# Kernel tuning notes

Hardware: AMD Instinct MI355X
Metric: run time of the kernel (lower is better)

The kernel has to match this reference:

```python
import jax, jax.numpy as jnp
import numpy as np

B, C, L, D = 8, 256, 2048, 128  # batch, in_channels, seq_len, n_factor


def setup_inputs() -> dict:
    key = jax.random.key(0)
    ks = jax.random.split(key, 8)
    s = 1.0 / np.sqrt(C)
    return {
        "x_inner": jax.random.normal(ks[0], (B, C, L), jnp.float32),
        "x_outer": jax.random.normal(ks[1], (B, C, L), jnp.float32),
        "Wq": jax.random.normal(ks[2], (D, C), jnp.float32) * s,
        "bq": jax.random.normal(ks[3], (D,), jnp.float32) * 0.01,
        "Wk": jax.random.normal(ks[4], (D, C), jnp.float32) * s,
        "bk": jax.random.normal(ks[5], (D,), jnp.float32) * 0.01,
        "Wv": jax.random.normal(ks[6], (D, C), jnp.float32) * s,
        "bv": jax.random.normal(ks[7], (D,), jnp.float32) * 0.01,
    }


def reference(x_inner, x_outer, Wq, bq, Wk, bk, Wv, bv):
    # kernel-size-1 Conv1d == per-position linear over channels; permute -> [B, L, D]
    q = jnp.einsum('bcl,dc->bld', x_inner, Wq) + bq  # [B, Lq, D]
    k = jnp.einsum('bcl,dc->bld', x_outer, Wk) + bk  # [B, Lk, D]
    v = jnp.einsum('bcl,dc->bld', x_outer, Wv) + bv  # [B, Lk, D]
    scores = jnp.einsum('bqd,bkd->bqk', q, k) / jnp.sqrt(jnp.asarray(D, q.dtype))
    attn = jax.nn.softmax(scores, axis=2)            # [B, Lq, Lk]
    return jnp.einsum('bqk,bkd->bqd', attn, v)       # [B, Lq, D]
```

## Files before the change

kernel.cpp:

```cpp
#include <hip/hip_runtime.h>
#include <hip/hip_bf16.h>

#define NB 8
#define NC 256
#define NL 2048
#define ND 128
#define NROWS (NB * NL)
#define QKV_ELEMS ((size_t)NB * NL * ND)
#define W_ELEMS (ND * NC)
#define XS_STRIDE 264

typedef __attribute__((ext_vector_type(8))) short bf16x8;
typedef __attribute__((ext_vector_type(4))) float f32x4;
typedef __attribute__((ext_vector_type(16))) float f32x16;

__device__ __forceinline__ unsigned short f2bf(float f) {
    union { float f; unsigned u; } v; v.f = f;
    unsigned r = v.u + 0x7fffu + ((v.u >> 16) & 1u);
    return (unsigned short)(r >> 16);
}

__device__ __forceinline__ void load_lds16(const unsigned short* g, unsigned short* l) {
    __builtin_amdgcn_global_load_lds((const __attribute__((address_space(1))) unsigned int*)g,
                                     (__attribute__((address_space(3))) unsigned int*)l, 16, 0, 0);
}

__global__ void cast_w3(const float* __restrict__ wq, const float* __restrict__ wk,
                        const float* __restrict__ wv, unsigned short* __restrict__ dst) {
    int i = blockIdx.x * blockDim.x + threadIdx.x;
    if (i >= 3 * W_ELEMS) return;
    int sel = i / W_ELEMS, off = i - sel * W_ELEMS;
    const float* s = (sel == 0) ? wq : (sel == 1) ? wk : wv;
    dst[i] = f2bf(s[off]);
}

__global__ __launch_bounds__(256, 4) void proj_direct(const float* __restrict__ xi,
                                                      const float* __restrict__ xo,
                                                      const unsigned short* __restrict__ Wall,
                                                      const float* __restrict__ bq,
                                                      const float* __restrict__ bk,
                                                      const float* __restrict__ bv,
                                                      unsigned short* __restrict__ Qb,
                                                      unsigned short* __restrict__ Kb,
                                                      unsigned short* __restrict__ Vtb) {
    __shared__ unsigned short xs[64 * XS_STRIDE];
    int b = blockIdx.x >> 5, lt = blockIdx.x & 31, l0 = lt * 64;
    int y = blockIdx.y;
    int wave = threadIdx.x >> 6, lane = threadIdx.x & 63;
    int ln = lane & 15, quad = lane >> 4;

    const float* xsrc = (y == 0 ? xi : xo) + (size_t)b * NC * NL + l0;
    int l4 = (lane & 15) * 4;
    int cr0 = wave * 4 + (lane >> 4);
    #pragma unroll
    for (int g = 0; g < 4; g++) {
        float4 r[4];
        #pragma unroll
        for (int gi = 0; gi < 4; gi++) {
            int c = cr0 + (g * 4 + gi) * 16;
            r[gi] = *reinterpret_cast<const float4*>(xsrc + (size_t)c * NL + l4);
        }
        #pragma unroll
        for (int gi = 0; gi < 4; gi++) {
            int c = cr0 + (g * 4 + gi) * 16;
            xs[(l4 + 0) * XS_STRIDE + c] = f2bf(r[gi].x);
            xs[(l4 + 1) * XS_STRIDE + c] = f2bf(r[gi].y);
            xs[(l4 + 2) * XS_STRIDE + c] = f2bf(r[gi].z);
            xs[(l4 + 3) * XS_STRIDE + c] = f2bf(r[gi].w);
        }
    }
    __syncthreads();

    if (y < 2) {
        const unsigned short* Wb = Wall + (size_t)y * W_ELEMS;
        const float* bias = y ? bk : bq;
        unsigned short* out = y ? Kb : Qb;
        int m0w = wave * 16;
        f32x4 acc[8] = {};
        #pragma unroll
        for (int s = 0; s < 8; s++) {
            bf16x8 af = *reinterpret_cast<const bf16x8*>(xs + (m0w + ln) * XS_STRIDE + s * 32 + quad * 8);
            #pragma unroll
            for (int t = 0; t < 8; t++) {
                bf16x8 bfr = *reinterpret_cast<const bf16x8*>(Wb + (size_t)(t * 16 + ln) * NC + s * 32 + quad * 8);
                acc[t] = __builtin_amdgcn_mfma_f32_16x16x32_bf16(af, bfr, acc[t], 0, 0, 0);
            }
        }
        #pragma unroll
        for (int t = 0; t < 8; t++) {
            int col = t * 16 + ln;
            float bi = bias[col];
            #pragma unroll
            for (int r = 0; r < 4; r++)
                out[(size_t)(b * NL + l0 + m0w + quad * 4 + r) * ND + col] = f2bf(acc[t][r] + bi);
        }
    } else {
        const unsigned short* Wb = Wall + 2 * (size_t)W_ELEMS;
        f32x4 acc[2][4] = {};
        #pragma unroll
        for (int s = 0; s < 8; s++) {
            bf16x8 wf0 = *reinterpret_cast<const bf16x8*>(Wb + (size_t)(wave * 32 + ln) * NC + s * 32 + quad * 8);
            bf16x8 wf1 = *reinterpret_cast<const bf16x8*>(Wb + (size_t)(wave * 32 + 16 + ln) * NC + s * 32 + quad * 8);
            #pragma unroll
            for (int t = 0; t < 4; t++) {
                bf16x8 xb = *reinterpret_cast<const bf16x8*>(xs + (t * 16 + ln) * XS_STRIDE + s * 32 + quad * 8);
                acc[0][t] = __builtin_amdgcn_mfma_f32_16x16x32_bf16(wf0, xb, acc[0][t], 0, 0, 0);
                acc[1][t] = __builtin_amdgcn_mfma_f32_16x16x32_bf16(wf1, xb, acc[1][t], 0, 0, 0);
            }
        }
        #pragma unroll
        for (int u = 0; u < 2; u++)
            #pragma unroll
            for (int t = 0; t < 4; t++)
                #pragma unroll
                for (int r = 0; r < 4; r++) {
                    int d = wave * 32 + u * 16 + quad * 4 + r;
                    Vtb[(size_t)(b * ND + d) * NL + l0 + t * 16 + ln] = f2bf(acc[u][t][r] + bv[d]);
                }
    }
}

__global__ __launch_bounds__(256, 2) void flash_attn_split(const unsigned short* __restrict__ Q,
                                                           const unsigned short* __restrict__ K,
                                                           const unsigned short* __restrict__ Vt,
                                                           float* __restrict__ Opart,
                                                           float* __restrict__ lbuf,
                                                           int kvlen) {
    __shared__ unsigned short kbuf[2][64 * 128];
    __shared__ unsigned short vbuf[2][128 * 64];
    __shared__ unsigned short pbuf[4][32 * 64];
    int b = blockIdx.x >> 4, qt = blockIdx.x & 15;
    int sp = blockIdx.y;
    int kv0 = sp * kvlen;
    int wave = threadIdx.x >> 6, lane = threadIdx.x & 63;
    int l31 = lane & 31, h = lane >> 5;
    int m0 = qt * 128 + wave * 32;
    const float scale = 0.08838834764831845f * 1.4426950408889634f;

    bf16x8 qf[8];
    const unsigned short* qrow = Q + (size_t)(b * NL + m0 + l31) * ND + h * 8;
    #pragma unroll
    for (int s = 0; s < 8; s++) qf[s] = *reinterpret_cast<const bf16x8*>(qrow + s * 16);

    float lsum = 0.f;
    f32x16 o_acc[4] = {};

    unsigned short* pw = pbuf[wave];
    const unsigned short* kg = K + (size_t)b * NL * ND;
    const unsigned short* vg = Vt + (size_t)b * ND * NL;

    int krt = wave * 16 + (lane >> 4);
    int kjs = (lane & 15);
    int vdt = wave * 32 + (lane >> 3);
    int vjs = (lane & 7);

    {
        int kt = kv0;
        #pragma unroll
        for (int i = 0; i < 4; i++) {
            int rt = krt + i * 4;
            load_lds16(kg + (size_t)(kt + rt) * ND + (kjs ^ (rt & 15)) * 8, kbuf[0] + (wave * 16 + i * 4) * 128);
        }
        #pragma unroll
        for (int i = 0; i < 4; i++) {
            int dt = vdt + i * 8;
            load_lds16(vg + (size_t)dt * NL + kt + (vjs ^ (dt & 7)) * 8, vbuf[0] + (wave * 32 + i * 8) * 64);
        }
    }

    int niter = kvlen >> 6;
    for (int it = 0; it < niter; it++) {
        int cur = it & 1;
        __syncthreads();

        if (it + 1 < niter) {
            int kt = kv0 + (it + 1) * 64;
            int nxt = cur ^ 1;
            #pragma unroll
            for (int i = 0; i < 4; i++) {
                int rt = krt + i * 4;
                load_lds16(kg + (size_t)(kt + rt) * ND + (kjs ^ (rt & 15)) * 8, kbuf[nxt] + (wave * 16 + i * 4) * 128);
            }
            #pragma unroll
            for (int i = 0; i < 4; i++) {
                int dt = vdt + i * 8;
                load_lds16(vg + (size_t)dt * NL + kt + (vjs ^ (dt & 7)) * 8, vbuf[nxt] + (wave * 32 + i * 8) * 64);
            }
        }
        const unsigned short* kb = kbuf[cur];
        const unsigned short* vb = vbuf[cur];

        f32x16 sacc[2] = {};
        #pragma unroll
        for (int tt = 0; tt < 2; tt++) {
            const unsigned short* krow_p = kb + (tt * 32 + l31) * 128;
            #pragma unroll
            for (int s = 0; s < 8; s++) {
                bf16x8 kf = *reinterpret_cast<const bf16x8*>(krow_p + (((s * 2 + h) ^ (lane & 15)) << 3));
                sacc[tt] = __builtin_amdgcn_mfma_f32_32x32x16_bf16(kf, qf[s], sacc[tt], 0, 0, 0);
            }
        }
        #pragma unroll
        for (int tt = 0; tt < 2; tt++) {
            #pragma unroll
            for (int g = 0; g < 4; g++) {
                float p0 = __builtin_exp2f(sacc[tt][g * 4 + 0] * scale);
                float p1 = __builtin_exp2f(sacc[tt][g * 4 + 1] * scale);
                float p2 = __builtin_exp2f(sacc[tt][g * 4 + 2] * scale);
                float p3 = __builtin_exp2f(sacc[tt][g * 4 + 3] * scale);
                lsum += (p0 + p1) + (p2 + p3);
                ushort4 o4 = { f2bf(p0), f2bf(p1), f2bf(p2), f2bf(p3) };
                int chunk = tt * 4 + g;
                *reinterpret_cast<ushort4*>(pw + l31 * 64 + ((chunk ^ (l31 & 7)) << 3) + h * 4) = o4;
            }
        }
        bf16x8 pb[4];
        #pragma unroll
        for (int step = 0; step < 4; step++)
            pb[step] = *reinterpret_cast<const bf16x8*>(pw + l31 * 64 + (((step * 2 + h) ^ (l31 & 7)) << 3));
        #pragma unroll
        for (int dt = 0; dt < 4; dt++) {
            const unsigned short* vrow = vb + (dt * 32 + l31) * 64;
            #pragma unroll
            for (int step = 0; step < 4; step++) {
                bf16x8 vf = *reinterpret_cast<const bf16x8*>(vrow + (((step * 2 + h) ^ (l31 & 7)) << 3));
                o_acc[dt] = __builtin_amdgcn_mfma_f32_32x32x16_bf16(vf, pb[step], o_acc[dt], 0, 0, 0);
            }
        }
    }
    lsum += __shfl_xor(lsum, 32);

    float* op = Opart + (size_t)sp * QKV_ELEMS;
    int qrow_g = b * NL + m0 + l31;
    if (lane < 32) lbuf[(size_t)sp * NROWS + qrow_g] = lsum;
    #pragma unroll
    for (int dt = 0; dt < 4; dt++) {
        #pragma unroll
        for (int g = 0; g < 4; g++) {
            f32x4 v4 = { o_acc[dt][g * 4 + 0], o_acc[dt][g * 4 + 1],
                         o_acc[dt][g * 4 + 2], o_acc[dt][g * 4 + 3] };
            *reinterpret_cast<f32x4*>(op + (size_t)qrow_g * ND + dt * 32 + g * 8 + h * 4) = v4;
        }
    }
}

__global__ __launch_bounds__(256) void attn_merge(const float* __restrict__ Opart,
                                                  const float* __restrict__ lbuf,
                                                  float* __restrict__ out, int S) {
    int idx = blockIdx.x * 256 + threadIdx.x;
    int row = idx >> 5;
    int dg = (idx & 31) * 4;
    float L = 0.f;
    float4 acc = make_float4(0.f, 0.f, 0.f, 0.f);
    for (int s = 0; s < S; s++) {
        L += lbuf[(size_t)s * NROWS + row];
        float4 o = *reinterpret_cast<const float4*>(Opart + (size_t)s * QKV_ELEMS + (size_t)row * ND + dg);
        acc.x += o.x; acc.y += o.y; acc.z += o.z; acc.w += o.w;
    }
    float inv = 1.0f / L;
    float4 res = make_float4(acc.x * inv, acc.y * inv, acc.z * inv, acc.w * inv);
    *reinterpret_cast<float4*>(out + (size_t)row * ND + dg) = res;
}

extern "C" void kernel_launch(void* const* d_in, const int* in_sizes, int n_in,
                              void* d_out, int out_size, void* d_ws, size_t ws_size,
                              hipStream_t stream) {
    const float* x_inner = (const float*)d_in[0];
    const float* x_outer = (const float*)d_in[1];
    const float* Wq = (const float*)d_in[2];
    const float* bq = (const float*)d_in[3];
    const float* Wk = (const float*)d_in[4];
    const float* bk = (const float*)d_in[5];
    const float* Wv = (const float*)d_in[6];
    const float* bv = (const float*)d_in[7];
    float* out = (float*)d_out;

    size_t need4 = 34078720u + 3 * QKV_ELEMS * 2 + 3 * W_ELEMS * 2;
    int S = (ws_size >= need4) ? 4 : 2;
    size_t union_bytes = (S == 4) ? 34078720u : 17039360u;

    char* w = (char*)d_ws;
    float* Opart = (float*)w;
    float* lbuf = (float*)(w + (size_t)S * QKV_ELEMS * 4);
    unsigned short* Qb = (unsigned short*)(w + union_bytes);
    unsigned short* Kb = Qb + QKV_ELEMS;
    unsigned short* Vtb = Kb + QKV_ELEMS;
    unsigned short* Wall = Vtb + QKV_ELEMS;

    cast_w3<<<(3 * W_ELEMS + 255) / 256, 256, 0, stream>>>(Wq, Wk, Wv, Wall);
    dim3 pgrid(NB * (NL / 64), 3);
    proj_direct<<<pgrid, 256, 0, stream>>>(x_inner, x_outer, Wall, bq, bk, bv, Qb, Kb, Vtb);
    dim3 fgrid(NB * (NL / 128), S);
    flash_attn_split<<<fgrid, 256, 0, stream>>>(Qb, Kb, Vtb, Opart, lbuf, NL / S);
    attn_merge<<<(NROWS * ND / 4 + 255) / 256, 256, 0, stream>>>(Opart, lbuf, out, S);
}
```

Measured before the change: 148.4 us.

## Fuse split-KV merge into attention via last-block atomic counter; packed bf16 casts

Removes the separate merge kernel. Each attention block increments a per-query-tile counter, and the last of the four split blocks sums the partial outputs and row sums and writes the normalized result. Float-to-bf16 conversions are also switched to a packed two-element intrinsic. This saves a kernel launch and its tail, but adds a memset launch, fences and atomics, and serializes the merge onto one block per tile. It also hardcodes four splits without checking the workspace size.

After: 198.1 us. +33.5%, slower.

```diff
diff --git a/kernel.cpp b/kernel.cpp
--- a/kernel.cpp
+++ b/kernel.cpp
@@ -9,6 +9,7 @@
 #define QKV_ELEMS ((size_t)NB * NL * ND)
 #define W_ELEMS (ND * NC)
 #define XS_STRIDE 264
+#define NSPLIT 4
 
 typedef __attribute__((ext_vector_type(8))) short bf16x8;
 typedef __attribute__((ext_vector_type(4))) float f32x4;
@@ -18,6 +19,11 @@
     union { float f; unsigned u; } v; v.f = f;
     unsigned r = v.u + 0x7fffu + ((v.u >> 16) & 1u);
     return (unsigned short)(r >> 16);
+}
+
+__device__ __forceinline__ unsigned f2bf_pk(float a, float b) {
+    __hip_bfloat162 h = __float22bfloat162_rn(make_float2(a, b));
+    return *reinterpret_cast<unsigned*>(&h);
 }
 
 __device__ __forceinline__ void load_lds16(const unsigned short* g, unsigned short* l) {
@@ -63,10 +69,12 @@
         #pragma unroll
         for (int gi = 0; gi < 4; gi++) {
             int c = cr0 + (g * 4 + gi) * 16;
-            xs[(l4 + 0) * XS_STRIDE + c] = f2bf(r[gi].x);
-            xs[(l4 + 1) * XS_STRIDE + c] = f2bf(r[gi].y);
-            xs[(l4 + 2) * XS_STRIDE + c] = f2bf(r[gi].z);
-            xs[(l4 + 3) * XS_STRIDE + c] = f2bf(r[gi].w);
+            unsigned pk0 = f2bf_pk(r[gi].x, r[gi].y);
+            unsigned pk1 = f2bf_pk(r[gi].z, r[gi].w);
+            xs[(l4 + 0) * XS_STRIDE + c] = (unsigned short)pk0;
+            xs[(l4 + 1) * XS_STRIDE + c] = (unsigned short)(pk0 >> 16);
+            xs[(l4 + 2) * XS_STRIDE + c] = (unsigned short)pk1;
+            xs[(l4 + 3) * XS_STRIDE + c] = (unsigned short)(pk1 >> 16);
         }
     }
     __syncthreads();
@@ -90,9 +98,13 @@
         for (int t = 0; t < 8; t++) {
             int col = t * 16 + ln;
             float bi = bias[col];
-            #pragma unroll
-            for (int r = 0; r < 4; r++)
-                out[(size_t)(b * NL + l0 + m0w + quad * 4 + r) * ND + col] = f2bf(acc[t][r] + bi);
+            unsigned pk0 = f2bf_pk(acc[t][0] + bi, acc[t][1] + bi);
+            unsigned pk1 = f2bf_pk(acc[t][2] + bi, acc[t][3] + bi);
+            size_t base = (size_t)(b * NL + l0 + m0w + quad * 4) * ND + col;
+            out[base + 0 * ND] = (unsigned short)pk0;
+            out[base + 1 * ND] = (unsigned short)(pk0 >> 16);
+            out[base + 2 * ND] = (unsigned short)pk1;
+            out[base + 3 * ND] = (unsigned short)(pk1 >> 16);
         }
     } else {
         const unsigned short* Wb = Wall + 2 * (size_t)W_ELEMS;
@@ -125,10 +137,13 @@
                                                            const unsigned short* __restrict__ Vt,
                                                            float* __restrict__ Opart,
                                                            float* __restrict__ lbuf,
+                                                           int* __restrict__ cnt,
+                                                           float* __restrict__ out,
                                                            int kvlen) {
     __shared__ unsigned short kbuf[2][64 * 128];
     __shared__ unsigned short vbuf[2][128 * 64];
     __shared__ unsigned short pbuf[4][32 * 64];
+    __shared__ int s_last;
     int b = blockIdx.x >> 4, qt = blockIdx.x & 15;
     int sp = blockIdx.y;
     int kv0 = sp * kvlen;
@@ -209,7 +224,9 @@
                 float p2 = __builtin_exp2f(sacc[tt][g * 4 + 2] * scale);
                 float p3 = __builtin_exp2f(sacc[tt][g * 4 + 3] * scale);
                 lsum += (p0 + p1) + (p2 + p3);
-                ushort4 o4 = { f2bf(p0), f2bf(p1), f2bf(p2), f2bf(p3) };
+                ushort4 o4;
+                *reinterpret_cast<unsigned*>(&o4.x) = f2bf_pk(p0, p1);
+                *reinterpret_cast<unsigned*>(&o4.z) = f2bf_pk(p2, p3);
                 int chunk = tt * 4 + g;
                 *reinterpret_cast<ushort4*>(pw + l31 * 64 + ((chunk ^ (l31 & 7)) << 3) + h * 4) = o4;
             }
@@ -242,24 +259,35 @@
             *reinterpret_cast<f32x4*>(op + (size_t)qrow_g * ND + dt * 32 + g * 8 + h * 4) = v4;
         }
     }
-}
-
-__global__ __launch_bounds__(256) void attn_merge(const float* __restrict__ Opart,
-                                                  const float* __restrict__ lbuf,
-                                                  float* __restrict__ out, int S) {
-    int idx = blockIdx.x * 256 + threadIdx.x;
-    int row = idx >> 5;
-    int dg = (idx & 31) * 4;
-    float L = 0.f;
-    float4 acc = make_float4(0.f, 0.f, 0.f, 0.f);
-    for (int s = 0; s < S; s++) {
-        L += lbuf[(size_t)s * NROWS + row];
-        float4 o = *reinterpret_cast<const float4*>(Opart + (size_t)s * QKV_ELEMS + (size_t)row * ND + dg);
-        acc.x += o.x; acc.y += o.y; acc.z += o.z; acc.w += o.w;
-    }
-    float inv = 1.0f / L;
-    float4 res = make_float4(acc.x * inv, acc.y * inv, acc.z * inv, acc.w * inv);
-    *reinterpret_cast<float4*>(out + (size_t)row * ND + dg) = res;
+
+    __syncthreads();
+    if (threadIdx.x == 0) {
+        __threadfence();
+        int old = atomicAdd(&cnt[blockIdx.x], 1);
+        s_last = (old == NSPLIT - 1);
+    }
+    __syncthreads();
+    if (s_last) {
+        __threadfence();
+        int row_local = threadIdx.x >> 1;
+        int d0 = (threadIdx.x & 1) * 64;
+        int g_row = b * NL + qt * 128 + row_local;
+        float L = 0.f;
+        #pragma unroll
+        for (int s = 0; s < NSPLIT; s++) L += lbuf[(size_t)s * NROWS + g_row];
+        float inv = 1.0f / L;
+        #pragma unroll
+        for (int j = 0; j < 16; j++) {
+            float4 a = make_float4(0.f, 0.f, 0.f, 0.f);
+            #pragma unroll
+            for (int s = 0; s < NSPLIT; s++) {
+                float4 o = *reinterpret_cast<const float4*>(Opart + (size_t)s * QKV_ELEMS + (size_t)g_row * ND + d0 + j * 4);
+                a.x += o.x; a.y += o.y; a.z += o.z; a.w += o.w;
+            }
+            float4 res = make_float4(a.x * inv, a.y * inv, a.z * inv, a.w * inv);
+            *reinterpret_cast<float4*>(out + (size_t)g_row * ND + d0 + j * 4) = res;
+        }
+    }
 }
 
 extern "C" void kernel_launch(void* const* d_in, const int* in_sizes, int n_in,
@@ -275,22 +303,20 @@
     const float* bv = (const float*)d_in[7];
     float* out = (float*)d_out;
 
-    size_t need4 = 34078720u + 3 * QKV_ELEMS * 2 + 3 * W_ELEMS * 2;
-    int S = (ws_size >= need4) ? 4 : 2;
-    size_t union_bytes = (S == 4) ? 34078720u : 17039360u;
-
+    size_t union_bytes = 34078720u;
     char* w = (char*)d_ws;
     float* Opart = (float*)w;
-    float* lbuf = (float*)(w + (size_t)S * QKV_ELEMS * 4);
+    float* lbuf = (float*)(w + (size_t)NSPLIT * QKV_ELEMS * 4);
     unsigned short* Qb = (unsigned short*)(w + union_bytes);
     unsigned short* Kb = Qb + QKV_ELEMS;
     unsigned short* Vtb = Kb + QKV_ELEMS;
     unsigned short* Wall = Vtb + QKV_ELEMS;
-
+    int* cnt = (int*)(Wall + 3 * W_ELEMS);
+
+    hipMemsetAsync(cnt, 0, NB * 16 * sizeof(int), stream);
     cast_w3<<<(3 * W_ELEMS + 255) / 256, 256, 0, stream>>>(Wq, Wk, Wv, Wall);
     dim3 pgrid(NB * (NL / 64), 3);
     proj_direct<<<pgrid, 256, 0, stream>>>(x_inner, x_outer, Wall, bq, bk, bv, Qb, Kb, Vtb);
-    dim3 fgrid(NB * (NL / 128), S);
-    flash_attn_split<<<fgrid, 256, 0, stream>>>(Qb, Kb, Vtb, Opart, lbuf, NL / S);
-    attn_merge<<<(NROWS * ND / 4 + 255) / 256, 256, 0, stream>>>(Opart, lbuf, out, S);
-}
+    dim3 fgrid(NB * (NL / 128), NSPLIT);
+    flash_attn_split<<<fgrid, 256, 0, stream>>>(Qb, Kb, Vtb, Opart, lbuf, cnt, out, NL / NSPLIT);
+}
```
